# Optimization experiments

Measured on AMD Instinct MI355X. Metric: run time of the kernel, lower is better.

Reference implementation:

```python
import jax, jax.numpy as jnp
import numpy as np

N_HEADS, INPUT_DIM, EMBED_DIM = 8, 128, 128
KEY_DIM = EMBED_DIM // N_HEADS  # val_dim = key_dim = 16
B, N = 8, 1024


def setup_inputs() -> dict:
    key = jax.random.key(0)
    ks = jax.random.split(key, 16)
    stdv_k = 1.0 / np.sqrt(KEY_DIM)
    stdv_e = 1.0 / np.sqrt(EMBED_DIM)

    def U(k, shape, s):
        return jax.random.uniform(k, shape, jnp.float32, -s, s)

    hdk = (N_HEADS, INPUT_DIM, KEY_DIM)
    hke = (N_HEADS, KEY_DIM, EMBED_DIM)
    return {
        "q_n": jax.random.normal(ks[0], (B, N, INPUT_DIM), jnp.float32),
        "q_c": jax.random.normal(ks[1], (B, N, INPUT_DIM), jnp.float32),
        "mask": jax.random.bernoulli(ks[2], 0.5, (B, N, N)),
        "W_query_n": U(ks[3], hdk, stdv_k),
        "W_key_nn": U(ks[4], hdk, stdv_k),
        "W_val_nn": U(ks[5], hdk, stdv_k),
        "W_key_c": U(ks[6], hdk, stdv_k),
        "W_val_c": U(ks[7], hdk, stdv_k),
        "W_query_c": U(ks[8], hdk, stdv_k),
        "W_key_n": U(ks[9], hdk, stdv_k),
        "W_val_n": U(ks[10], hdk, stdv_k),
        "W_out_node": U(ks[11], hke, stdv_e),
        "W_out_color": U(ks[12], hke, stdv_e),
    }


def reference(q_n, q_c, mask, W_query_n, W_key_nn, W_val_nn, W_key_c, W_val_c,
              W_query_c, W_key_n, W_val_n, W_out_node, W_out_color):
    norm = 1.0 / jnp.sqrt(jnp.asarray(KEY_DIM, q_n.dtype))
    neg_inf = jnp.asarray(-jnp.inf, q_n.dtype)

    def proj(x, W):  # (B,N,D), (H,D,K) -> (H,B,N,K)
        return jnp.einsum('bnd,hdk->hbnk', x, W)

    # --- color stream: q_c attends over nodes q_n ---
    Q_c = proj(q_c, W_query_c)
    K_n = proj(q_n, W_key_n)
    V_n = proj(q_n, W_val_n)
    attn_c = jax.nn.softmax(norm * jnp.einsum('hbqk,hbnk->hbqn', Q_c, K_n), axis=-1)
    heads_c = jnp.einsum('hbqn,hbnv->hbqv', attn_c, V_n)
    out_color = jnp.einsum('hbqv,hve->bqe', heads_c, W_out_color)

    # --- node stream: masked self-attention + attention over colors ---
    Q_n = proj(q_n, W_query_n)
    K_nn = proj(q_n, W_key_nn)
    V_nn = proj(q_n, W_val_nn)
    comp_nn = norm * jnp.einsum('hbqk,hbnk->hbqn', Q_n, K_nn)
    m = mask[None]  # (1,B,Q,N) broadcast over heads; True = not allowed
    comp_nn = jnp.where(m, neg_inf, comp_nn)
    attn_nn = jax.nn.softmax(comp_nn, axis=-1)
    attn_nn = jnp.where(m, jnp.asarray(0.0, q_n.dtype), attn_nn)
    heads_nn = jnp.einsum('hbqn,hbnv->hbqv', attn_nn, V_nn)

    K_nc = proj(q_c, W_key_c)
    V_nc = proj(q_c, W_val_c)
    attn_nc = jax.nn.softmax(norm * jnp.einsum('hbqk,hbnk->hbqn', Q_n, K_nc), axis=-1)
    heads_nc = jnp.einsum('hbqn,hbnv->hbqv', attn_nc, V_nc)

    heads = heads_nn + heads_nc
    out = jnp.einsum('hbqv,hve->bqe', heads, W_out_node)
    return (out, out_color)
```

## Files before the change

kernel.cpp:

```cpp
#include <hip/hip_runtime.h>
#include <stdint.h>

#define NH 8
#define NB 8
#define NN 1024
#define ND 128
#define NK 16
#define NF (NB*NN)
#define C2EXP 0.36067376022224085f
#define LSTR 136

typedef float f32x16 __attribute__((ext_vector_type(16)));
typedef short bf16x8 __attribute__((ext_vector_type(8)));

__device__ __forceinline__ uint16_t f2bf(float f){
  uint32_t x = __float_as_uint(f);
  uint32_t r = (x + 0x7fffu + ((x>>16)&1u)) >> 16;
  return (uint16_t)r;
}
__device__ __forceinline__ float fast_exp2(float x){
#if __has_builtin(__builtin_amdgcn_exp2f)
  return __builtin_amdgcn_exp2f(x);
#else
  return exp2f(x);
#endif
}

__global__ __launch_bounds__(256) void pack_kernel(const int* __restrict__ mask,
                                                   uint32_t* __restrict__ packN,
                                                   uint16_t* __restrict__ onesw){
  if (blockIdx.x == 0) {
    for (int i = threadIdx.x; i < 1024; i += 256) onesw[i] = 0x3F80;
  }
  const int w = threadIdx.x >> 6, lane = threadIdx.x & 63;
  const int row = blockIdx.x*4 + w;
  const int* mp = mask + (size_t)row*NN;
  uint32_t* dst = packN + (size_t)row*32;
  for (int wq = 0; wq < 16; ++wq) {
    int v = mp[wq*64 + lane];
    unsigned long long bal = __ballot(v != 0);
    if (lane == 0) { dst[wq*2] = (uint32_t)bal; dst[wq*2+1] = (uint32_t)(bal>>32); }
  }
}

struct ProjArgs { const float* x[8]; const float* w[8]; };

__global__ __launch_bounds__(256) void proj_kernel(ProjArgs args, uint16_t* ws){
  __shared__ __align__(16) uint16_t WT[128*LSTR];
  __shared__ __align__(16) uint16_t S[128*LSTR];
  const int p = blockIdx.y;
  const int rb = blockIdx.x;
  const int tid = threadIdx.x;

  const float4* w4 = (const float4*)args.w[p];
  #pragma unroll
  for (int i = 0; i < 16; ++i) {
    int e4 = i*256 + tid;
    float4 f = w4[e4];
    int e = e4*4;
    int h = e >> 11, d = (e >> 4) & 127, k = e & 15;
    uint16_t* wr = &WT[(h*16 + k)*LSTR + d];
    wr[0*LSTR] = f2bf(f.x); wr[1*LSTR] = f2bf(f.y);
    wr[2*LSTR] = f2bf(f.z); wr[3*LSTR] = f2bf(f.w);
  }
  __syncthreads();

  const int wave = tid >> 6, lane = tid & 63;
  const int l5 = lane >> 5, lm = lane & 31;
  const int r0 = rb*128 + wave*32;
  const float* xrow = args.x[p] + (size_t)(r0 + lm)*ND + l5*8;

  bf16x8 afr[8];
  #pragma unroll
  for (int kt = 0; kt < 8; ++kt) {
    float4 f0 = *(const float4*)(xrow + kt*16);
    float4 f1 = *(const float4*)(xrow + kt*16 + 4);
    bf16x8 a;
    a[0]=f2bf(f0.x); a[1]=f2bf(f0.y); a[2]=f2bf(f0.z); a[3]=f2bf(f0.w);
    a[4]=f2bf(f1.x); a[5]=f2bf(f1.y); a[6]=f2bf(f1.z); a[7]=f2bf(f1.w);
    afr[kt] = a;
  }

  const bool tr = (p==2)|(p==5)|(p==7);
  const float qsc = (p==0 || p==3) ? C2EXP : 1.0f;
  #pragma unroll
  for (int nt = 0; nt < 4; ++nt) {
    f32x16 acc;
    #pragma unroll
    for (int i = 0; i < 16; ++i) acc[i] = 0.f;
    #pragma unroll
    for (int kt = 0; kt < 8; ++kt) {
      bf16x8 b = *(const bf16x8*)(&WT[(nt*32 + lm)*LSTR + kt*16 + l5*8]);
      acc = __builtin_amdgcn_mfma_f32_32x32x16_bf16(afr[kt], b, acc, 0, 0, 0);
    }
    #pragma unroll
    for (int i = 0; i < 16; ++i) {
      int r = wave*32 + (i&3) + 8*(i>>2) + 4*l5;
      int c = nt*32 + lm;
      if (tr) {
        int t2 = (r>>2)&3;
        int rp = (t2==1 || t2==2) ? (r^12) : r;
        S[c*LSTR + rp] = f2bf(acc[i]);
      } else {
        S[r*LSTR + c] = f2bf(acc[i]*qsc);
      }
    }
  }
  __syncthreads();

  uint16_t* dst = ws + (size_t)p*((size_t)NH*NF*NK);
  if (!tr) {
    #pragma unroll
    for (int it = 0; it < 8; ++it) {
      int c = it*256 + tid;
      int row = c >> 4, cg = c & 15;
      bf16x8 v = *(const bf16x8*)(&S[row*LSTR + cg*8]);
      int h = cg >> 1, k8 = cg & 1;
      *(bf16x8*)(dst + ((size_t)h*NF + rb*128 + row)*NK + k8*8) = v;
    }
  } else {
    const int b = rb >> 3, nb = (rb & 7)*128;
    #pragma unroll
    for (int it = 0; it < 8; ++it) {
      int c = it*256 + tid;
      int col = c >> 4, ng = c & 15;
      bf16x8 v = *(const bf16x8*)(&S[col*LSTR + ng*8]);
      int h = col >> 4, k = col & 15;
      *(bf16x8*)(dst + ((size_t)(h*NB + b)*NK + k)*NN + nb + ng*8) = v;
    }
  }
}

template<bool MASKED>
__device__ __forceinline__ void attn_stream(
    const uint4* __restrict__ kbuf, bf16x8 aq,
    const uint16_t* __restrict__ vbase, const uint4* __restrict__ pmw4,
    int nh, int l5, int lm, f32x16& O)
{
  f32x16 Z;
  #pragma unroll
  for (int i = 0; i < 16; ++i) Z[i] = 0.f;

  uint32_t mw[16];
  if (MASKED) {
    uint4 m0 = pmw4[nh*4+0], m1 = pmw4[nh*4+1];
    uint4 m2 = pmw4[nh*4+2], m3 = pmw4[nh*4+3];
    mw[0]=m0.x; mw[1]=m0.y; mw[2]=m0.z; mw[3]=m0.w;
    mw[4]=m1.x; mw[5]=m1.y; mw[6]=m1.z; mw[7]=m1.w;
    mw[8]=m2.x; mw[9]=m2.y; mw[10]=m2.z; mw[11]=m2.w;
    mw[12]=m3.x; mw[13]=m3.y; mw[14]=m3.z; mw[15]=m3.w;
  }

  const int base_n = nh*512;
  const bool vload = (lm < 17);

  bf16x8 av1, av2, av1n, av2n;
  #pragma unroll
  for (int i = 0; i < 8; ++i) { av1[i]=0; av2[i]=0; av1n[i]=0; av2n[i]=0; }
  if (vload) {
    const uint16_t* vp = vbase + base_n + l5*8;
    av1 = *(const bf16x8*)(vp);
    av2 = *(const bf16x8*)(vp + 16);
  }
  f32x16 Stc = __builtin_amdgcn_mfma_f32_32x32x16_bf16(
      *(const bf16x8*)(&kbuf[l5*1024 + base_n + lm]), aq, Z, 0, 0, 0);

  #pragma unroll
  for (int t = 0; t < 16; ++t) {
    f32x16 Stn;
    if (t < 15) {
      const int n1 = base_n + (t+1)*32;
      if (vload) {
        const uint16_t* vp = vbase + n1 + l5*8;
        av1n = *(const bf16x8*)(vp);
        av2n = *(const bf16x8*)(vp + 16);
      }
      Stn = __builtin_amdgcn_mfma_f32_32x32x16_bf16(
          *(const bf16x8*)(&kbuf[l5*1024 + n1 + lm]), aq, Z, 0, 0, 0);
    }

    const uint32_t mws = MASKED ? (mw[t] >> (4*l5)) : 0u;
    float p[16];
    #pragma unroll
    for (int i = 0; i < 16; ++i) {
      float pv = fast_exp2(Stc[i]);
      if (MASKED && ((mws >> ((i&3) + 8*(i>>2))) & 1u)) pv = 0.f;
      p[i] = pv;
    }
    union { uint32_t u[4]; bf16x8 v; } B1, B2;
    #pragma unroll
    for (int k = 0; k < 4; ++k) {
      B1.u[k] = __builtin_amdgcn_perm(__float_as_uint(p[2*k+1]),
                                      __float_as_uint(p[2*k]),   0x07060302u);
      B2.u[k] = __builtin_amdgcn_perm(__float_as_uint(p[2*k+9]),
                                      __float_as_uint(p[2*k+8]), 0x07060302u);
    }
    O = __builtin_amdgcn_mfma_f32_32x32x16_bf16(av1, B1.v, O, 0, 0, 0);
    O = __builtin_amdgcn_mfma_f32_32x32x16_bf16(av2, B2.v, O, 0, 0, 0);

    if (t < 15) { Stc = Stn; av1 = av1n; av2 = av2n; }
  }
}

__global__ __launch_bounds__(512, 4) void attn_kernel(
    const uint16_t* __restrict__ Qn_, const uint16_t* __restrict__ K1n,
    const uint16_t* __restrict__ V1n, const uint16_t* __restrict__ K2n,
    const uint16_t* __restrict__ V2n,
    const uint16_t* __restrict__ Qc_, const uint16_t* __restrict__ K1c,
    const uint16_t* __restrict__ V1c,
    const uint32_t* __restrict__ packN, const uint16_t* __restrict__ onesb,
    uint16_t* __restrict__ hn_, uint16_t* __restrict__ hc_)
{
  __shared__ uint4 kbuf[2048];
  const bool dual = (blockIdx.z == 0);
  const uint16_t* Q   = dual ? Qn_ : Qc_;
  const uint16_t* K1  = dual ? K1n : K1c;
  uint16_t* outp      = dual ? hn_ : hc_;

  const int hb = blockIdx.y;
  const int h = hb >> 3, b = hb & 7;
  const size_t base = ((size_t)h*NF + (size_t)b*NN)*NK;
  const int tid = threadIdx.x;

  const uint4* k1 = (const uint4*)(K1 + base);
  for (int i = tid; i < 2048; i += 512)
    kbuf[(i & 1)*1024 + (i >> 1)] = k1[i];
  __syncthreads();

  const int wave = tid >> 6, lane = tid & 63;
  const int l5 = lane >> 5, lm = lane & 31;
  const int qt = wave & 3, nh = wave >> 2;
  const int q = blockIdx.x*128 + qt*32 + lm;

  const bf16x8 aq = *(const bf16x8*)(Q + base + (size_t)q*NK + l5*8);
  const uint4* pmw4 = (const uint4*)(packN + ((size_t)b*NN + q)*32);

  const uint16_t* VT1 = (dual ? V1n : V1c) + (size_t)hb*(NK*NN);
  const uint16_t* vb1 = (lm < 16) ? (VT1 + (size_t)lm*NN) : onesb;

  f32x16 O1, O2;
  #pragma unroll
  for (int i = 0; i < 16; ++i) { O1[i] = 0.f; O2[i] = 0.f; }

  if (dual) {
    attn_stream<true>(kbuf, aq, vb1, pmw4, nh, l5, lm, O1);
    __syncthreads();
    const uint4* k2 = (const uint4*)(K2n + base);
    for (int i = tid; i < 2048; i += 512)
      kbuf[(i & 1)*1024 + (i >> 1)] = k2[i];
    __syncthreads();
    const uint16_t* VT2 = V2n + (size_t)hb*(NK*NN);
    const uint16_t* vb2 = (lm < 16) ? (VT2 + (size_t)lm*NN) : onesb;
    attn_stream<false>(kbuf, aq, vb2, nullptr, nh, l5, lm, O2);
  } else {
    attn_stream<false>(kbuf, aq, vb1, nullptr, nh, l5, lm, O1);
  }

  float L1 = O1[8] + __shfl_xor(O1[8], 32, 64);
  float L2 = O2[8] + __shfl_xor(O2[8], 32, 64);

  __syncthreads();
  float* cw = ((float*)kbuf) + ((size_t)(qt*2 + l5)*32 + lm)*18;
  if (nh == 1) {
    #pragma unroll
    for (int i = 0; i < 8; ++i) cw[i] = O1[i];
    if (dual) {
      #pragma unroll
      for (int i = 0; i < 8; ++i) cw[8+i] = O2[i];
    }
    cw[16] = L1; cw[17] = L2;
  }
  __syncthreads();
  if (nh == 0) {
    const float l1 = L1 + cw[16];
    const float i1 = (l1 > 0.f) ? 1.f/l1 : 0.f;
    float i2 = 0.f;
    if (dual) { const float l2 = L2 + cw[17]; i2 = (l2 > 0.f) ? 1.f/l2 : 0.f; }
    uint32_t w[4];
    #pragma unroll
    for (int k = 0; k < 4; ++k) {
      float va = (O1[2*k]   + cw[2*k])  *i1;
      float vb = (O1[2*k+1] + cw[2*k+1])*i1;
      if (dual) { va += (O2[2*k] + cw[8+2*k])*i2; vb += (O2[2*k+1] + cw[8+2*k+1])*i2; }
      w[k] = ((uint32_t)f2bf(vb) << 16) | f2bf(va);
    }
    uint16_t* hp = outp + ((size_t)b*NN + q)*128 + h*16 + l5*4;
    *(uint2*)(hp)     = make_uint2(w[0], w[1]);
    *(uint2*)(hp + 8) = make_uint2(w[2], w[3]);
  }
}

__global__ __launch_bounds__(256) void outproj_kernel(
    const uint16_t* __restrict__ hn, const uint16_t* __restrict__ hc,
    const float* __restrict__ wn, const float* __restrict__ wc,
    float* __restrict__ out)
{
  __shared__ __align__(16) uint16_t WT[128*LSTR];
  const int s = blockIdx.y;
  const int rb = blockIdx.x;
  const int tid = threadIdx.x;
  const float* wsrc = s ? wc : wn;
  const float4* w4 = (const float4*)wsrc;
  #pragma unroll
  for (int i = 0; i < 16; ++i) {
    int e4 = i*256 + tid;
    float4 f = w4[e4];
    int e = e4*4;
    int c = e >> 7, col = e & 127;
    uint16_t* wr = &WT[col*LSTR + c];
    wr[0*LSTR] = f2bf(f.x); wr[1*LSTR] = f2bf(f.y);
    wr[2*LSTR] = f2bf(f.z); wr[3*LSTR] = f2bf(f.w);
  }
  __syncthreads();

  const int wave = tid >> 6, lane = tid & 63;
  const int l5 = lane >> 5, lm = lane & 31;
  const int rt = wave & 1, nh2 = wave >> 1;
  const int r0 = rb*64 + rt*32;
  const uint16_t* hp = (s ? hc : hn) + (size_t)(r0 + lm)*128 + l5*8;
  bf16x8 afr[8];
  #pragma unroll
  for (int kt = 0; kt < 8; ++kt) afr[kt] = *(const bf16x8*)(hp + kt*16);

  float* dst = out + (size_t)s*((size_t)NF*ND) + (size_t)r0*ND;
  #pragma unroll
  for (int nt2 = 0; nt2 < 2; ++nt2) {
    const int nt = nh2*2 + nt2;
    f32x16 acc;
    #pragma unroll
    for (int i = 0; i < 16; ++i) acc[i] = 0.f;
    #pragma unroll
    for (int kt = 0; kt < 8; ++kt) {
      bf16x8 b = *(const bf16x8*)(&WT[(nt*32 + lm)*LSTR + kt*16 + l5*8]);
      acc = __builtin_amdgcn_mfma_f32_32x32x16_bf16(afr[kt], b, acc, 0, 0, 0);
    }
    #pragma unroll
    for (int i = 0; i < 16; ++i) {
      int r = (i&3) + 8*(i>>2) + 4*l5;
      dst[(size_t)r*ND + nt*32 + lm] = acc[i];
    }
  }
}

extern "C" void kernel_launch(void* const* d_in, const int* in_sizes, int n_in,
                              void* d_out, int out_size, void* d_ws, size_t ws_size,
                              hipStream_t stream)
{
  const float* q_n = (const float*)d_in[0];
  const float* q_c = (const float*)d_in[1];
  const int* mask = (const int*)d_in[2];
  const float* W[10];
  for (int i = 0; i < 10; ++i) W[i] = (const float*)d_in[3+i];

  uint16_t* ws16 = (uint16_t*)d_ws;
  const size_t PE = (size_t)NH*NF*NK;
  uint16_t* Qc   = ws16 + 0*PE;
  uint16_t* Kn   = ws16 + 1*PE;
  uint16_t* VTn  = ws16 + 2*PE;
  uint16_t* Qn   = ws16 + 3*PE;
  uint16_t* Knn  = ws16 + 4*PE;
  uint16_t* VTnn = ws16 + 5*PE;
  uint16_t* Knc  = ws16 + 6*PE;
  uint16_t* VTnc = ws16 + 7*PE;
  uint16_t* heads_node = ws16 + 8*PE;
  uint32_t* packN   = (uint32_t*)(ws16 + 9*PE);
  uint16_t* heads_c = ws16 + 10*PE;
  uint16_t* onesb   = ws16 + 11*PE;

  pack_kernel<<<2048, 256, 0, stream>>>(mask, packN, onesb);

  ProjArgs pa;
  pa.x[0]=q_c; pa.w[0]=W[5];
  pa.x[1]=q_n; pa.w[1]=W[6];
  pa.x[2]=q_n; pa.w[2]=W[7];
  pa.x[3]=q_n; pa.w[3]=W[0];
  pa.x[4]=q_n; pa.w[4]=W[1];
  pa.x[5]=q_n; pa.w[5]=W[2];
  pa.x[6]=q_c; pa.w[6]=W[3];
  pa.x[7]=q_c; pa.w[7]=W[4];
  proj_kernel<<<dim3(64, 8), 256, 0, stream>>>(pa, ws16);

  attn_kernel<<<dim3(8, 64, 2), 512, 0, stream>>>(
      Qn, Knn, VTnn, Knc, VTnc, Qc, Kn, VTn, packN, onesb,
      heads_node, heads_c);

  outproj_kernel<<<dim3(128, 2), 256, 0, stream>>>(heads_node, heads_c,
                                                   W[8], W[9], (float*)d_out);
}
```

Baseline: 165.2 us.

## Split node-stream dual attention into separate blocks, sum heads in outproj

The node stream previously ran both the masked self-attention and the attention over colors back to back in one block, so those blocks did twice the work of the color-stream blocks. This change launches a third grid slice so each block handles a single attention. The two node partial head outputs are written separately and summed inside the output projection by issuing a second MFMA per k-step. It aims to balance load and add parallelism, at the cost of an extra bf16 workspace buffer, extra global traffic, and rounding each partial to bf16 before the sum.

After: 167.4 us. About the same (+1.4%).

```diff
diff --git a/kernel.cpp b/kernel.cpp
--- a/kernel.cpp
+++ b/kernel.cpp
@@ -203,28 +203,30 @@
 }
 
 __global__ __launch_bounds__(512, 4) void attn_kernel(
-    const uint16_t* __restrict__ Qn_, const uint16_t* __restrict__ K1n,
-    const uint16_t* __restrict__ V1n, const uint16_t* __restrict__ K2n,
-    const uint16_t* __restrict__ V2n,
-    const uint16_t* __restrict__ Qc_, const uint16_t* __restrict__ K1c,
-    const uint16_t* __restrict__ V1c,
+    const uint16_t* __restrict__ Qn_, const uint16_t* __restrict__ Qc_,
+    const uint16_t* __restrict__ Knn, const uint16_t* __restrict__ VTnn,
+    const uint16_t* __restrict__ Knc, const uint16_t* __restrict__ VTnc,
+    const uint16_t* __restrict__ Knc_c, const uint16_t* __restrict__ VTc,
     const uint32_t* __restrict__ packN, const uint16_t* __restrict__ onesb,
-    uint16_t* __restrict__ hn_, uint16_t* __restrict__ hc_)
+    uint16_t* __restrict__ h_nn, uint16_t* __restrict__ h_nc,
+    uint16_t* __restrict__ h_c)
 {
   __shared__ uint4 kbuf[2048];
-  const bool dual = (blockIdx.z == 0);
-  const uint16_t* Q   = dual ? Qn_ : Qc_;
-  const uint16_t* K1  = dual ? K1n : K1c;
-  uint16_t* outp      = dual ? hn_ : hc_;
+  const int z = blockIdx.z;
+  const bool masked = (z == 0);
+  const uint16_t* Q  = (z == 2) ? Qc_ : Qn_;
+  const uint16_t* K  = (z == 0) ? Knn : (z == 1) ? Knc : Knc_c;
+  const uint16_t* VT = (z == 0) ? VTnn : (z == 1) ? VTnc : VTc;
+  uint16_t* outp     = (z == 0) ? h_nn : (z == 1) ? h_nc : h_c;
 
   const int hb = blockIdx.y;
   const int h = hb >> 3, b = hb & 7;
   const size_t base = ((size_t)h*NF + (size_t)b*NN)*NK;
   const int tid = threadIdx.x;
 
-  const uint4* k1 = (const uint4*)(K1 + base);
+  const uint4* kg = (const uint4*)(K + base);
   for (int i = tid; i < 2048; i += 512)
-    kbuf[(i & 1)*1024 + (i >> 1)] = k1[i];
+    kbuf[(i & 1)*1024 + (i >> 1)] = kg[i];
   __syncthreads();
 
   const int wave = tid >> 6, lane = tid & 63;
@@ -235,54 +237,35 @@
   const bf16x8 aq = *(const bf16x8*)(Q + base + (size_t)q*NK + l5*8);
   const uint4* pmw4 = (const uint4*)(packN + ((size_t)b*NN + q)*32);
 
-  const uint16_t* VT1 = (dual ? V1n : V1c) + (size_t)hb*(NK*NN);
-  const uint16_t* vb1 = (lm < 16) ? (VT1 + (size_t)lm*NN) : onesb;
-
-  f32x16 O1, O2;
-  #pragma unroll
-  for (int i = 0; i < 16; ++i) { O1[i] = 0.f; O2[i] = 0.f; }
-
-  if (dual) {
-    attn_stream<true>(kbuf, aq, vb1, pmw4, nh, l5, lm, O1);
-    __syncthreads();
-    const uint4* k2 = (const uint4*)(K2n + base);
-    for (int i = tid; i < 2048; i += 512)
-      kbuf[(i & 1)*1024 + (i >> 1)] = k2[i];
-    __syncthreads();
-    const uint16_t* VT2 = V2n + (size_t)hb*(NK*NN);
-    const uint16_t* vb2 = (lm < 16) ? (VT2 + (size_t)lm*NN) : onesb;
-    attn_stream<false>(kbuf, aq, vb2, nullptr, nh, l5, lm, O2);
-  } else {
-    attn_stream<false>(kbuf, aq, vb1, nullptr, nh, l5, lm, O1);
-  }
-
-  float L1 = O1[8] + __shfl_xor(O1[8], 32, 64);
-  float L2 = O2[8] + __shfl_xor(O2[8], 32, 64);
-
-  __syncthreads();
-  float* cw = ((float*)kbuf) + ((size_t)(qt*2 + l5)*32 + lm)*18;
+  const uint16_t* VTb = VT + (size_t)hb*(NK*NN);
+  const uint16_t* vb = (lm < 16) ? (VTb + (size_t)lm*NN) : onesb;
+
+  f32x16 O;
+  #pragma unroll
+  for (int i = 0; i < 16; ++i) O[i] = 0.f;
+
+  if (masked) attn_stream<true >(kbuf, aq, vb, pmw4, nh, l5, lm, O);
+  else        attn_stream<false>(kbuf, aq, vb, nullptr, nh, l5, lm, O);
+
+  float L = O[8] + __shfl_xor(O[8], 32, 64);
+
+  __syncthreads();
+  float* cw = ((float*)kbuf) + ((size_t)(qt*2 + l5)*32 + lm)*10;
   if (nh == 1) {
     #pragma unroll
-    for (int i = 0; i < 8; ++i) cw[i] = O1[i];
-    if (dual) {
-      #pragma unroll
-      for (int i = 0; i < 8; ++i) cw[8+i] = O2[i];
-    }
-    cw[16] = L1; cw[17] = L2;
+    for (int i = 0; i < 8; ++i) cw[i] = O[i];
+    cw[8] = L;
   }
   __syncthreads();
   if (nh == 0) {
-    const float l1 = L1 + cw[16];
-    const float i1 = (l1 > 0.f) ? 1.f/l1 : 0.f;
-    float i2 = 0.f;
-    if (dual) { const float l2 = L2 + cw[17]; i2 = (l2 > 0.f) ? 1.f/l2 : 0.f; }
+    const float l = L + cw[8];
+    const float il = (l > 0.f) ? 1.f/l : 0.f;
     uint32_t w[4];
     #pragma unroll
     for (int k = 0; k < 4; ++k) {
-      float va = (O1[2*k]   + cw[2*k])  *i1;
-      float vb = (O1[2*k+1] + cw[2*k+1])*i1;
-      if (dual) { va += (O2[2*k] + cw[8+2*k])*i2; vb += (O2[2*k+1] + cw[8+2*k+1])*i2; }
-      w[k] = ((uint32_t)f2bf(vb) << 16) | f2bf(va);
+      float va = (O[2*k]   + cw[2*k])  *il;
+      float vb2 = (O[2*k+1] + cw[2*k+1])*il;
+      w[k] = ((uint32_t)f2bf(vb2) << 16) | f2bf(va);
     }
     uint16_t* hp = outp + ((size_t)b*NN + q)*128 + h*16 + l5*4;
     *(uint2*)(hp)     = make_uint2(w[0], w[1]);
@@ -291,7 +274,8 @@
 }
 
 __global__ __launch_bounds__(256) void outproj_kernel(
-    const uint16_t* __restrict__ hn, const uint16_t* __restrict__ hc,
+    const uint16_t* __restrict__ hnn, const uint16_t* __restrict__ hnc,
+    const uint16_t* __restrict__ hc,
     const float* __restrict__ wn, const float* __restrict__ wc,
     float* __restrict__ out)
 {
@@ -317,10 +301,15 @@
   const int l5 = lane >> 5, lm = lane & 31;
   const int rt = wave & 1, nh2 = wave >> 1;
   const int r0 = rb*64 + rt*32;
-  const uint16_t* hp = (s ? hc : hn) + (size_t)(r0 + lm)*128 + l5*8;
-  bf16x8 afr[8];
-  #pragma unroll
-  for (int kt = 0; kt < 8; ++kt) afr[kt] = *(const bf16x8*)(hp + kt*16);
+  const size_t hoff = (size_t)(r0 + lm)*128 + l5*8;
+  const uint16_t* hp1 = (s ? hc : hnn) + hoff;
+  const uint16_t* hp2 = hnc + hoff;
+  bf16x8 afr1[8], afr2[8];
+  #pragma unroll
+  for (int kt = 0; kt < 8; ++kt) {
+    afr1[kt] = *(const bf16x8*)(hp1 + kt*16);
+    if (!s) afr2[kt] = *(const bf16x8*)(hp2 + kt*16);
+  }
 
   float* dst = out + (size_t)s*((size_t)NF*ND) + (size_t)r0*ND;
   #pragma unroll
@@ -332,7 +321,9 @@
     #pragma unroll
     for (int kt = 0; kt < 8; ++kt) {
       bf16x8 b = *(const bf16x8*)(&WT[(nt*32 + lm)*LSTR + kt*16 + l5*8]);
-      acc = __builtin_amdgcn_mfma_f32_32x32x16_bf16(afr[kt], b, acc, 0, 0, 0);
+      acc = __builtin_amdgcn_mfma_f32_32x32x16_bf16(afr1[kt], b, acc, 0, 0, 0);
+      if (!s)
+        acc = __builtin_amdgcn_mfma_f32_32x32x16_bf16(afr2[kt], b, acc, 0, 0, 0);
     }
     #pragma unroll
     for (int i = 0; i < 16; ++i) {
@@ -362,10 +353,11 @@
   uint16_t* VTnn = ws16 + 5*PE;
   uint16_t* Knc  = ws16 + 6*PE;
   uint16_t* VTnc = ws16 + 7*PE;
-  uint16_t* heads_node = ws16 + 8*PE;
+  uint16_t* heads_nn = ws16 + 8*PE;
   uint32_t* packN   = (uint32_t*)(ws16 + 9*PE);
-  uint16_t* heads_c = ws16 + 10*PE;
-  uint16_t* onesb   = ws16 + 11*PE;
+  uint16_t* heads_c  = ws16 + 10*PE;
+  uint16_t* heads_nc = ws16 + 11*PE;
+  uint16_t* onesb    = ws16 + 12*PE;
 
   pack_kernel<<<2048, 256, 0, stream>>>(mask, packN, onesb);
 
@@ -380,10 +372,10 @@
   pa.x[7]=q_c; pa.w[7]=W[4];
   proj_kernel<<<dim3(64, 8), 256, 0, stream>>>(pa, ws16);
 
-  attn_kernel<<<dim3(8, 64, 2), 512, 0, stream>>>(
-      Qn, Knn, VTnn, Knc, VTnc, Qc, Kn, VTn, packN, onesb,
-      heads_node, heads_c);
-
-  outproj_kernel<<<dim3(128, 2), 256, 0, stream>>>(heads_node, heads_c,
+  attn_kernel<<<dim3(8, 64, 3), 512, 0, stream>>>(
+      Qn, Qc, Knn, VTnn, Knc, VTnc, Kn, VTn, packN, onesb,
+      heads_nn, heads_nc, heads_c);
+
+  outproj_kernel<<<dim3(128, 2), 256, 0, stream>>>(heads_nn, heads_nc, heads_c,
                                                    W[8], W[9], (float*)d_out);
 }
```
